# Kernel tuning notes

Hardware: AMD Instinct MI355X
Metric: run time of the kernel (lower is better)

Reference implementation:

```python
import jax, jax.numpy as jnp
import numpy as np

N, F, P, O, E = 20000, 8, 12, 32, 320000


def setup_inputs() -> dict:
    key = jax.random.key(0)
    ks = jax.random.split(key, 18)
    g = lambda k, shape: (jax.random.normal(k, shape, jnp.float32) * 0.1)
    x = jax.random.normal(ks[0], (N, F, P), jnp.float32)
    edge_index = jax.random.randint(ks[1], (2, E), 0, N, dtype=jnp.int32)
    return {
        "x": x,
        "edge_index": edge_index,
        # GCNConv weights/biases for update (z), reset (r), candidate (h) gates
        "Wz": g(ks[2], (F, O)), "bz": g(ks[3], (O,)),
        "Wr": g(ks[4], (F, O)), "br": g(ks[5], (O,)),
        "Wh": g(ks[6], (F, O)), "bh": g(ks[7], (O,)),
        # GRU linear layers (torch.nn.Linear: y = x @ W.T + b), in=2*O, out=O
        "lz_w": g(ks[8], (O, 2 * O)), "lz_b": g(ks[9], (O,)),
        "lr_w": g(ks[10], (O, 2 * O)), "lr_b": g(ks[11], (O,)),
        "lh_w": g(ks[12], (O, 2 * O)), "lh_b": g(ks[13], (O,)),
        # temporal attention logits over periods
        "att": g(ks[14], (P,)),
        # final Linear(32 -> window_size)
        "out_w": g(ks[15], (P, O)), "out_b": g(ks[16], (P,)),
    }


def reference(x, edge_index, Wz, bz, Wr, br, Wh, bh,
              lz_w, lz_b, lr_w, lr_b, lh_w, lh_b, att, out_w, out_b):
    n = x.shape[0]
    # gcn_norm with self-loops: norm_e = d^-1/2[src] * d^-1/2[dst]
    loop = jnp.arange(n, dtype=edge_index.dtype)
    src = jnp.concatenate([edge_index[0], loop])
    dst = jnp.concatenate([edge_index[1], loop])
    deg = jax.ops.segment_sum(jnp.ones(src.shape[0], x.dtype), dst, num_segments=n)
    dinv = jnp.where(deg > 0, deg ** -0.5, 0.0)
    norm = dinv[src] * dinv[dst]  # [E+n]

    def gcn(xp, W, b):
        # xp: [n, P, F] -> [n, P, O]; GCNConv: D^-1/2 (A+I) D^-1/2 (X W) + b
        h = jnp.einsum('npf,fo->npo', xp, W)
        msg = h[src] * norm[:, None, None]  # [E+n, P, O]
        return jax.ops.segment_sum(msg, dst, num_segments=n) + b

    xp = jnp.transpose(x, (0, 2, 1))  # [n, P, F]
    # A3TGCN does NOT carry H across periods (H stays initial zeros), so all
    # periods are independent GRU steps from H = 0 and can be batched.
    H = jnp.zeros(xp.shape[:2] + (O,), x.dtype)
    Z = jax.nn.sigmoid(jnp.concatenate([gcn(xp, Wz, bz), H], -1) @ lz_w.T + lz_b)
    R = jax.nn.sigmoid(jnp.concatenate([gcn(xp, Wr, br), H], -1) @ lr_w.T + lr_b)
    Ht = jnp.tanh(jnp.concatenate([gcn(xp, Wh, bh), H * R], -1) @ lh_w.T + lh_b)
    Hp = Z * H + (1.0 - Z) * Ht  # [n, P, O]
    probs = jax.nn.softmax(att)
    Hacc = jnp.einsum('npo,p->no', Hp, probs)  # attention-weighted sum
    return jax.nn.relu(Hacc) @ out_w.T + out_b  # [n, window_size]
```

## Files before the change

### kernel.cpp

```cpp
#include <hip/hip_runtime.h>
#include <math.h>

#define FP 96
#define SLOT 64
#define NPB 8
#define GBLK 128
#define PBLK 256
#define POISON ((int)0xAAAAAAAA)

__device__ __forceinline__ unsigned f2bf_bits(float f) {
    unsigned u = __float_as_uint(f);
    return (u + 0x7fffu + ((u >> 16) & 1u)) >> 16;
}
__device__ __forceinline__ float bf_lo(unsigned u) { return __uint_as_float(u << 16); }
__device__ __forceinline__ float bf_hi(unsigned u) { return __uint_as_float(u & 0xffff0000u); }

__device__ __forceinline__ int cnt_decode(int v) {
    return ((unsigned)v >= 0xAA000000u) ? v - POISON : v;
}

__global__ void k_hist_fold(const int* __restrict__ ei, int E,
                            int* __restrict__ cnt, int* __restrict__ bucket,
                            const float* __restrict__ Wz, const float* __restrict__ bz,
                            const float* __restrict__ Wh, const float* __restrict__ bh,
                            const float* __restrict__ lz_w, const float* __restrict__ lz_b,
                            const float* __restrict__ lh_w, const float* __restrict__ lh_b,
                            const float* __restrict__ att, const float* __restrict__ out_w,
                            const float* __restrict__ out_b, float* __restrict__ cst) {
    int b = blockIdx.x, t = threadIdx.x;
    if (b == gridDim.x - 1) {
        int f = t >> 5, o = t & 31;
        float sz = 0.f, sh = 0.f;
        for (int j = 0; j < 32; ++j) {
            sz += Wz[f * 32 + j] * lz_w[o * 64 + j];
            sh += Wh[f * 32 + j] * lh_w[o * 64 + j];
        }
        cst[t]       = sz;
        cst[256 + t] = sh;
        if (t < 32) {
            float a = lz_b[t], c = lh_b[t];
            for (int j = 0; j < 32; ++j) {
                a += bz[j] * lz_w[t * 64 + j];
                c += bh[j] * lh_w[t * 64 + j];
            }
            cst[512 + t] = a;
            cst[544 + t] = c;
        }
        if (t < 12) {
            float m = -1e30f;
            for (int p = 0; p < 12; ++p) m = fmaxf(m, att[p]);
            float s = 0.f;
            for (int p = 0; p < 12; ++p) s += expf(att[p] - m);
            cst[576 + t] = expf(att[t] - m) / s;
        }
        for (int i = t; i < 384; i += PBLK)
            cst[588 + (i & 31) * 12 + (i >> 5)] = out_w[i];
        if (t < 12) cst[972 + t] = out_b[t];
        return;
    }
    int e = b * PBLK + t;
    if (e >= E) return;
    int src = ei[e], dst = ei[E + e];
    int old = atomicAdd(cnt + dst, 1);
    int pos = cnt_decode(old);
    if (pos < SLOT) bucket[(size_t)dst * SLOT + pos] = src;
}

__global__ void k_convert(const float* __restrict__ x, const int* __restrict__ cnt,
                          unsigned* __restrict__ xb, int N) {
    int i = blockIdx.x * blockDim.x + threadIdx.x;
    if (i >= (N + 1) * 12) return;
    int n = i / 12;
    if (n == N) {
        ((uint4*)xb)[i] = make_uint4(0u, 0u, 0u, 0u);
        return;
    }
    int deg = cnt_decode(cnt[n]);
    float w = rsqrtf((float)(deg + 1));
    const float4* x4 = (const float4*)x;
    float4 a = x4[i * 2], c = x4[i * 2 + 1];
    uint4 r;
    r.x = f2bf_bits(w * a.x) | (f2bf_bits(w * a.y) << 16);
    r.y = f2bf_bits(w * a.z) | (f2bf_bits(w * a.w) << 16);
    r.z = f2bf_bits(w * c.x) | (f2bf_bits(w * c.y) << 16);
    r.w = f2bf_bits(w * c.z) | (f2bf_bits(w * c.w) << 16);
    ((uint4*)xb)[i] = r;
}

__device__ __forceinline__ void load_batch(uint4* P, const uint4* __restrict__ xrow,
                                           const int* list, int k) {
#pragma unroll
    for (int u = 0; u < 8; ++u) P[u] = xrow[list[u] * 12 + k];
}
__device__ __forceinline__ void acc_batch(float* acc, const uint4* C) {
    acc[0] += ((bf_lo(C[0].x) + bf_lo(C[1].x)) + (bf_lo(C[2].x) + bf_lo(C[3].x)))
            + ((bf_lo(C[4].x) + bf_lo(C[5].x)) + (bf_lo(C[6].x) + bf_lo(C[7].x)));
    acc[1] += ((bf_hi(C[0].x) + bf_hi(C[1].x)) + (bf_hi(C[2].x) + bf_hi(C[3].x)))
            + ((bf_hi(C[4].x) + bf_hi(C[5].x)) + (bf_hi(C[6].x) + bf_hi(C[7].x)));
    acc[2] += ((bf_lo(C[0].y) + bf_lo(C[1].y)) + (bf_lo(C[2].y) + bf_lo(C[3].y)))
            + ((bf_lo(C[4].y) + bf_lo(C[5].y)) + (bf_lo(C[6].y) + bf_lo(C[7].y)));
    acc[3] += ((bf_hi(C[0].y) + bf_hi(C[1].y)) + (bf_hi(C[2].y) + bf_hi(C[3].y)))
            + ((bf_hi(C[4].y) + bf_hi(C[5].y)) + (bf_hi(C[6].y) + bf_hi(C[7].y)));
    acc[4] += ((bf_lo(C[0].z) + bf_lo(C[1].z)) + (bf_lo(C[2].z) + bf_lo(C[3].z)))
            + ((bf_lo(C[4].z) + bf_lo(C[5].z)) + (bf_lo(C[6].z) + bf_lo(C[7].z)));
    acc[5] += ((bf_hi(C[0].z) + bf_hi(C[1].z)) + (bf_hi(C[2].z) + bf_hi(C[3].z)))
            + ((bf_hi(C[4].z) + bf_hi(C[5].z)) + (bf_hi(C[6].z) + bf_hi(C[7].z)));
    acc[6] += ((bf_lo(C[0].w) + bf_lo(C[1].w)) + (bf_lo(C[2].w) + bf_lo(C[3].w)))
            + ((bf_lo(C[4].w) + bf_lo(C[5].w)) + (bf_lo(C[6].w) + bf_lo(C[7].w)));
    acc[7] += ((bf_hi(C[0].w) + bf_hi(C[1].w)) + (bf_hi(C[2].w) + bf_hi(C[3].w)))
            + ((bf_hi(C[4].w) + bf_hi(C[5].w)) + (bf_hi(C[6].w) + bf_hi(C[7].w)));
}

__global__ void __launch_bounds__(GBLK)
k_gather_gates(const unsigned* __restrict__ xb, const int* __restrict__ cnt,
               const int* __restrict__ bucket, const float* __restrict__ cst,
               float* __restrict__ out, int N) {
    __shared__ float sy[NPB][FP + 4];
    __shared__ float shr[NPB][32];
    __shared__ float scst[984];
    __shared__ int   sbuck[NPB][72];
    __shared__ int   sdeg[NPB];
    int t = threadIdx.x;
    int n0 = blockIdx.x * NPB;
    const uint4* xrow = (const uint4*)xb;

    int nl = 0, k = 0, n = N;
    uint4 self = make_uint4(0u, 0u, 0u, 0u);
    if (t < NPB * 12) {
        nl = t / 12; k = t - nl * 12; n = n0 + nl;
        if (n < N) self = xrow[n * 12 + k];
    }
    if (t < NPB) sdeg[t] = (n0 + t < N) ? cnt_decode(cnt[n0 + t]) : 0;
    {
        int nd = t >> 4, q = t & 15, nn = n0 + nd;
        if (nn < N) *(int4*)&sbuck[nd][q * 4] =
            ((const int4*)(bucket + (size_t)nn * SLOT))[q];
    }
    for (int i = t; i < 984; i += GBLK) scst[i] = cst[i];
    __syncthreads();
    if (t < NPB * 8) {
        int nnl = t >> 3, q = t & 7;
        int d = min(sdeg[nnl], SLOT);
        int degp = (d + 7) & ~7; if (degp < 8) degp = 8;
        int pos = d + q;
        if (pos < degp) sbuck[nnl][pos] = N;
    }
    __syncthreads();

    if (t < NPB * 12 && n < N) {
        int c = sdeg[nl];
        int d = min(c, SLOT);
        int degp = (d + 7) & ~7; if (degp < 8) degp = 8;
        int nb = degp >> 3;
        int nA = (nb + 1) >> 1;
        int nB = nb - nA;
        const int* list = sbuck[nl];
        float acc[8] = {bf_lo(self.x), bf_hi(self.x), bf_lo(self.y), bf_hi(self.y),
                        bf_lo(self.z), bf_hi(self.z), bf_lo(self.w), bf_hi(self.w)};
        uint4 A[8], B[8];
        load_batch(A, xrow, list, k);
        if (nB > 0) load_batch(B, xrow, list + nA * 8, k);
        for (int i = 0; i < nA; ++i) {
            uint4 CA[8];
#pragma unroll
            for (int u = 0; u < 8; ++u) CA[u] = A[u];
            if (i + 1 < nA) load_batch(A, xrow, list + (i + 1) * 8, k);
            acc_batch(acc, CA);
            if (i < nB) {
                uint4 CB[8];
#pragma unroll
                for (int u = 0; u < 8; ++u) CB[u] = B[u];
                if (i + 1 < nB) load_batch(B, xrow, list + (nA + i + 1) * 8, k);
                acc_batch(acc, CB);
            }
        }
        float di = rsqrtf((float)(c + 1));
#pragma unroll
        for (int i = 0; i < 8; ++i) sy[nl][k * 8 + i] = di * acc[i];
    }
    __syncthreads();

    int o = t & 31;
#pragma unroll
    for (int it = 0; it < 2; ++it) {
        int local = (t >> 5) + it * 4, nn = n0 + local;
        if (nn < N) {
            float cz = scst[512 + o], ch = scst[544 + o];
            float hacc = 0.f;
#pragma unroll
            for (int p = 0; p < 12; ++p) {
                float az = cz, ah = ch;
#pragma unroll
                for (int f = 0; f < 8; ++f) {
                    float xf = sy[local][f * 12 + p];
                    az += xf * scst[f * 32 + o];
                    ah += xf * scst[256 + f * 32 + o];
                }
                float Z  = 1.f / (1.f + expf(-az));
                float Ht = tanhf(ah);
                hacc += scst[576 + p] * (1.f - Z) * Ht;
            }
            shr[local][o] = fmaxf(hacc, 0.f);
        }
    }
    __syncthreads();
#pragma unroll
    for (int it = 0; it < 2; ++it) {
        int local = (t >> 5) + it * 4, nn = n0 + local;
        if (nn < N && o < 12) {
            float s = scst[972 + o];
#pragma unroll
            for (int j2 = 0; j2 < 32; ++j2)
                s += shr[local][j2] * scst[588 + j2 * 12 + o];
            out[(size_t)nn * 12 + o] = s;
        }
    }
}

extern "C" void kernel_launch(void* const* d_in, const int* in_sizes, int n_in,
                              void* d_out, int out_size, void* d_ws, size_t ws_size,
                              hipStream_t stream) {
    const float* x    = (const float*)d_in[0];
    const int*   ei   = (const int*)d_in[1];
    const float* Wz   = (const float*)d_in[2];
    const float* bz   = (const float*)d_in[3];
    const float* Wh   = (const float*)d_in[6];
    const float* bh   = (const float*)d_in[7];
    const float* lz_w = (const float*)d_in[8];
    const float* lz_b = (const float*)d_in[9];
    const float* lh_w = (const float*)d_in[12];
    const float* lh_b = (const float*)d_in[13];
    const float* att  = (const float*)d_in[14];
    const float* ow   = (const float*)d_in[15];
    const float* ob   = (const float*)d_in[16];
    float* out = (float*)d_out;

    int N = in_sizes[0] / FP;
    int E = in_sizes[1] / 2;

    int*      cnt    = (int*)d_ws;
    int*      bucket = cnt + N;
    unsigned* xb     = (unsigned*)(bucket + (size_t)N * SLOT);
    float*    cst    = (float*)(xb + (size_t)(N + 1) * 48);

    int EB = (E + PBLK - 1) / PBLK;
    k_hist_fold<<<EB + 1, PBLK, 0, stream>>>(ei, E, cnt, bucket, Wz, bz, Wh, bh,
                                             lz_w, lz_b, lh_w, lh_b, att, ow, ob, cst);
    k_convert  <<<((N + 1) * 12 + PBLK - 1) / PBLK, PBLK, 0, stream>>>(x, cnt, xb, N);
    k_gather_gates<<<(N + NPB - 1) / NPB, GBLK, 0, stream>>>(xb, cnt, bucket, cst, out, N);
}
```

Measured before the change: 140.0 us.

## Fuse bf16 conversion into histogram kernel and apply source norm during gather

The bf16 conversion of x no longer scales rows by the source degree, so it can run in the same launch as the edge histogram and constant folding. This removes one kernel launch and the serial dependency between the histogram and the conversion. The gather kernel now loads each neighbour's count and applies rsqrt(deg+1) per neighbour with FMAs. The cost is an extra random int load and rsqrt per edge in the hot gather loop, plus more register pressure. The count array grows by one entry so the padding index N can be read safely.

```diff
diff --git a/kernel.cpp b/kernel.cpp
--- a/kernel.cpp
+++ b/kernel.cpp
@@ -19,96 +19,94 @@
     return ((unsigned)v >= 0xAA000000u) ? v - POISON : v;
 }
 
-__global__ void k_hist_fold(const int* __restrict__ ei, int E,
-                            int* __restrict__ cnt, int* __restrict__ bucket,
-                            const float* __restrict__ Wz, const float* __restrict__ bz,
-                            const float* __restrict__ Wh, const float* __restrict__ bh,
-                            const float* __restrict__ lz_w, const float* __restrict__ lz_b,
-                            const float* __restrict__ lh_w, const float* __restrict__ lh_b,
-                            const float* __restrict__ att, const float* __restrict__ out_w,
-                            const float* __restrict__ out_b, float* __restrict__ cst) {
+__global__ void k_prep_all(const int* __restrict__ ei, int E, int EB, int CB,
+                           int* __restrict__ cnt, int* __restrict__ bucket,
+                           const float* __restrict__ x, unsigned* __restrict__ xb, int N,
+                           const float* __restrict__ Wz, const float* __restrict__ bz,
+                           const float* __restrict__ Wh, const float* __restrict__ bh,
+                           const float* __restrict__ lz_w, const float* __restrict__ lz_b,
+                           const float* __restrict__ lh_w, const float* __restrict__ lh_b,
+                           const float* __restrict__ att, const float* __restrict__ out_w,
+                           const float* __restrict__ out_b, float* __restrict__ cst) {
     int b = blockIdx.x, t = threadIdx.x;
-    if (b == gridDim.x - 1) {
-        int f = t >> 5, o = t & 31;
-        float sz = 0.f, sh = 0.f;
+    if (b < EB) {
+        int e = b * PBLK + t;
+        if (e >= E) return;
+        int src = ei[e], dst = ei[E + e];
+        int old = atomicAdd(cnt + dst, 1);
+        int pos = cnt_decode(old);
+        if (pos < SLOT) bucket[(size_t)dst * SLOT + pos] = src;
+        return;
+    }
+    if (b < EB + CB) {
+        int i = (b - EB) * PBLK + t;
+        if (i >= (N + 1) * 12) return;
+        if (i / 12 == N) {
+            ((uint4*)xb)[i] = make_uint4(0u, 0u, 0u, 0u);
+            return;
+        }
+        const float4* x4 = (const float4*)x;
+        float4 a = x4[i * 2], c = x4[i * 2 + 1];
+        uint4 r;
+        r.x = f2bf_bits(a.x) | (f2bf_bits(a.y) << 16);
+        r.y = f2bf_bits(a.z) | (f2bf_bits(a.w) << 16);
+        r.z = f2bf_bits(c.x) | (f2bf_bits(c.y) << 16);
+        r.w = f2bf_bits(c.z) | (f2bf_bits(c.w) << 16);
+        ((uint4*)xb)[i] = r;
+        return;
+    }
+    int f = t >> 5, o = t & 31;
+    float sz = 0.f, sh = 0.f;
+    for (int j = 0; j < 32; ++j) {
+        sz += Wz[f * 32 + j] * lz_w[o * 64 + j];
+        sh += Wh[f * 32 + j] * lh_w[o * 64 + j];
+    }
+    cst[t]       = sz;
+    cst[256 + t] = sh;
+    if (t < 32) {
+        float a = lz_b[t], c = lh_b[t];
         for (int j = 0; j < 32; ++j) {
-            sz += Wz[f * 32 + j] * lz_w[o * 64 + j];
-            sh += Wh[f * 32 + j] * lh_w[o * 64 + j];
-        }
-        cst[t]       = sz;
-        cst[256 + t] = sh;
-        if (t < 32) {
-            float a = lz_b[t], c = lh_b[t];
-            for (int j = 0; j < 32; ++j) {
-                a += bz[j] * lz_w[t * 64 + j];
-                c += bh[j] * lh_w[t * 64 + j];
-            }
-            cst[512 + t] = a;
-            cst[544 + t] = c;
-        }
-        if (t < 12) {
-            float m = -1e30f;
-            for (int p = 0; p < 12; ++p) m = fmaxf(m, att[p]);
-            float s = 0.f;
-            for (int p = 0; p < 12; ++p) s += expf(att[p] - m);
-            cst[576 + t] = expf(att[t] - m) / s;
-        }
-        for (int i = t; i < 384; i += PBLK)
-            cst[588 + (i & 31) * 12 + (i >> 5)] = out_w[i];
-        if (t < 12) cst[972 + t] = out_b[t];
-        return;
-    }
-    int e = b * PBLK + t;
-    if (e >= E) return;
-    int src = ei[e], dst = ei[E + e];
-    int old = atomicAdd(cnt + dst, 1);
-    int pos = cnt_decode(old);
-    if (pos < SLOT) bucket[(size_t)dst * SLOT + pos] = src;
-}
-
-__global__ void k_convert(const float* __restrict__ x, const int* __restrict__ cnt,
-                          unsigned* __restrict__ xb, int N) {
-    int i = blockIdx.x * blockDim.x + threadIdx.x;
-    if (i >= (N + 1) * 12) return;
-    int n = i / 12;
-    if (n == N) {
-        ((uint4*)xb)[i] = make_uint4(0u, 0u, 0u, 0u);
-        return;
-    }
-    int deg = cnt_decode(cnt[n]);
-    float w = rsqrtf((float)(deg + 1));
-    const float4* x4 = (const float4*)x;
-    float4 a = x4[i * 2], c = x4[i * 2 + 1];
-    uint4 r;
-    r.x = f2bf_bits(w * a.x) | (f2bf_bits(w * a.y) << 16);
-    r.y = f2bf_bits(w * a.z) | (f2bf_bits(w * a.w) << 16);
-    r.z = f2bf_bits(w * c.x) | (f2bf_bits(w * c.y) << 16);
-    r.w = f2bf_bits(w * c.z) | (f2bf_bits(w * c.w) << 16);
-    ((uint4*)xb)[i] = r;
-}
-
-__device__ __forceinline__ void load_batch(uint4* P, const uint4* __restrict__ xrow,
+            a += bz[j] * lz_w[t * 64 + j];
+            c += bh[j] * lh_w[t * 64 + j];
+        }
+        cst[512 + t] = a;
+        cst[544 + t] = c;
+    }
+    if (t < 12) {
+        float m = -1e30f;
+        for (int p = 0; p < 12; ++p) m = fmaxf(m, att[p]);
+        float s = 0.f;
+        for (int p = 0; p < 12; ++p) s += expf(att[p] - m);
+        cst[576 + t] = expf(att[t] - m) / s;
+    }
+    for (int i = t; i < 384; i += PBLK)
+        cst[588 + (i & 31) * 12 + (i >> 5)] = out_w[i];
+    if (t < 12) cst[972 + t] = out_b[t];
+}
+
+__device__ __forceinline__ void load_batch(uint4* P, int* pc, const uint4* __restrict__ xrow,
+                                           const int* __restrict__ cntp,
                                            const int* list, int k) {
 #pragma unroll
-    for (int u = 0; u < 8; ++u) P[u] = xrow[list[u] * 12 + k];
-}
-__device__ __forceinline__ void acc_batch(float* acc, const uint4* C) {
-    acc[0] += ((bf_lo(C[0].x) + bf_lo(C[1].x)) + (bf_lo(C[2].x) + bf_lo(C[3].x)))
-            + ((bf_lo(C[4].x) + bf_lo(C[5].x)) + (bf_lo(C[6].x) + bf_lo(C[7].x)));
-    acc[1] += ((bf_hi(C[0].x) + bf_hi(C[1].x)) + (bf_hi(C[2].x) + bf_hi(C[3].x)))
-            + ((bf_hi(C[4].x) + bf_hi(C[5].x)) + (bf_hi(C[6].x) + bf_hi(C[7].x)));
-    acc[2] += ((bf_lo(C[0].y) + bf_lo(C[1].y)) + (bf_lo(C[2].y) + bf_lo(C[3].y)))
-            + ((bf_lo(C[4].y) + bf_lo(C[5].y)) + (bf_lo(C[6].y) + bf_lo(C[7].y)));
-    acc[3] += ((bf_hi(C[0].y) + bf_hi(C[1].y)) + (bf_hi(C[2].y) + bf_hi(C[3].y)))
-            + ((bf_hi(C[4].y) + bf_hi(C[5].y)) + (bf_hi(C[6].y) + bf_hi(C[7].y)));
-    acc[4] += ((bf_lo(C[0].z) + bf_lo(C[1].z)) + (bf_lo(C[2].z) + bf_lo(C[3].z)))
-            + ((bf_lo(C[4].z) + bf_lo(C[5].z)) + (bf_lo(C[6].z) + bf_lo(C[7].z)));
-    acc[5] += ((bf_hi(C[0].z) + bf_hi(C[1].z)) + (bf_hi(C[2].z) + bf_hi(C[3].z)))
-            + ((bf_hi(C[4].z) + bf_hi(C[5].z)) + (bf_hi(C[6].z) + bf_hi(C[7].z)));
-    acc[6] += ((bf_lo(C[0].w) + bf_lo(C[1].w)) + (bf_lo(C[2].w) + bf_lo(C[3].w)))
-            + ((bf_lo(C[4].w) + bf_lo(C[5].w)) + (bf_lo(C[6].w) + bf_lo(C[7].w)));
-    acc[7] += ((bf_hi(C[0].w) + bf_hi(C[1].w)) + (bf_hi(C[2].w) + bf_hi(C[3].w)))
-            + ((bf_hi(C[4].w) + bf_hi(C[5].w)) + (bf_hi(C[6].w) + bf_hi(C[7].w)));
+    for (int u = 0; u < 8; ++u) {
+        int s = list[u];
+        pc[u] = cntp[s];
+        P[u]  = xrow[s * 12 + k];
+    }
+}
+__device__ __forceinline__ void acc_batch_w(float* acc, const uint4* C, const int* pc) {
+#pragma unroll
+    for (int u = 0; u < 8; ++u) {
+        float w = rsqrtf((float)(cnt_decode(pc[u]) + 1));
+        acc[0] = fmaf(w, bf_lo(C[u].x), acc[0]);
+        acc[1] = fmaf(w, bf_hi(C[u].x), acc[1]);
+        acc[2] = fmaf(w, bf_lo(C[u].y), acc[2]);
+        acc[3] = fmaf(w, bf_hi(C[u].y), acc[3]);
+        acc[4] = fmaf(w, bf_lo(C[u].z), acc[4]);
+        acc[5] = fmaf(w, bf_hi(C[u].z), acc[5]);
+        acc[6] = fmaf(w, bf_lo(C[u].w), acc[6]);
+        acc[7] = fmaf(w, bf_hi(C[u].w), acc[7]);
+    }
 }
 
 __global__ void __launch_bounds__(GBLK)
@@ -155,26 +153,29 @@
         int nA = (nb + 1) >> 1;
         int nB = nb - nA;
         const int* list = sbuck[nl];
-        float acc[8] = {bf_lo(self.x), bf_hi(self.x), bf_lo(self.y), bf_hi(self.y),
-                        bf_lo(self.z), bf_hi(self.z), bf_lo(self.w), bf_hi(self.w)};
+        float di = rsqrtf((float)(c + 1));
+        float acc[8] = {di * bf_lo(self.x), di * bf_hi(self.x),
+                        di * bf_lo(self.y), di * bf_hi(self.y),
+                        di * bf_lo(self.z), di * bf_hi(self.z),
+                        di * bf_lo(self.w), di * bf_hi(self.w)};
         uint4 A[8], B[8];
-        load_batch(A, xrow, list, k);
-        if (nB > 0) load_batch(B, xrow, list + nA * 8, k);
+        int   cA[8], cB[8];
+        load_batch(A, cA, xrow, cnt, list, k);
+        if (nB > 0) load_batch(B, cB, xrow, cnt, list + nA * 8, k);
         for (int i = 0; i < nA; ++i) {
-            uint4 CA[8];
-#pragma unroll
-            for (int u = 0; u < 8; ++u) CA[u] = A[u];
-            if (i + 1 < nA) load_batch(A, xrow, list + (i + 1) * 8, k);
-            acc_batch(acc, CA);
+            uint4 CA[8]; int wA[8];
+#pragma unroll
+            for (int u = 0; u < 8; ++u) { CA[u] = A[u]; wA[u] = cA[u]; }
+            if (i + 1 < nA) load_batch(A, cA, xrow, cnt, list + (i + 1) * 8, k);
+            acc_batch_w(acc, CA, wA);
             if (i < nB) {
-                uint4 CB[8];
-#pragma unroll
-                for (int u = 0; u < 8; ++u) CB[u] = B[u];
-                if (i + 1 < nB) load_batch(B, xrow, list + (nA + i + 1) * 8, k);
-                acc_batch(acc, CB);
+                uint4 CB[8]; int wB[8];
+#pragma unroll
+                for (int u = 0; u < 8; ++u) { CB[u] = B[u]; wB[u] = cB[u]; }
+                if (i + 1 < nB) load_batch(B, cB, xrow, cnt, list + (nA + i + 1) * 8, k);
+                acc_batch_w(acc, CB, wB);
             }
         }
-        float di = rsqrtf((float)(c + 1));
 #pragma unroll
         for (int i = 0; i < 8; ++i) sy[nl][k * 8 + i] = di * acc[i];
     }
@@ -239,13 +240,14 @@
     int E = in_sizes[1] / 2;
 
     int*      cnt    = (int*)d_ws;
-    int*      bucket = cnt + N;
+    int*      bucket = cnt + (N + 1);
     unsigned* xb     = (unsigned*)(bucket + (size_t)N * SLOT);
     float*    cst    = (float*)(xb + (size_t)(N + 1) * 48);
 
     int EB = (E + PBLK - 1) / PBLK;
-    k_hist_fold<<<EB + 1, PBLK, 0, stream>>>(ei, E, cnt, bucket, Wz, bz, Wh, bh,
-                                             lz_w, lz_b, lh_w, lh_b, att, ow, ob, cst);
-    k_convert  <<<((N + 1) * 12 + PBLK - 1) / PBLK, PBLK, 0, stream>>>(x, cnt, xb, N);
+    int CB = ((N + 1) * 12 + PBLK - 1) / PBLK;
+    k_prep_all<<<EB + CB + 1, PBLK, 0, stream>>>(ei, E, EB, CB, cnt, bucket, x, xb, N,
+                                                 Wz, bz, Wh, bh, lz_w, lz_b, lh_w, lh_b,
+                                                 att, ow, ob, cst);
     k_gather_gates<<<(N + NPB - 1) / NPB, GBLK, 0, stream>>>(xb, cnt, bucket, cst, out, N);
 }
```

Result: slower. 144.0 us (+2.8%).

## Split per-node neighbor gather across two thread halves and double block size

Applied to the files above, without the earlier changes.

Doubles the gather block to 256 threads and assigns two threads per (node, feature-chunk), each gathering half of the padded neighbor list into separate shared buffers that are then summed. This is meant to shorten the serial per-thread gather chain and raise memory-level parallelism in the latency-bound neighbor loads. The gate stage now runs one node per 32-thread group instead of looping twice. It costs an extra shared-memory reduction pass, a barrier, more padding to multiples of 16, and higher register and LDS pressure per block. The bucket pointer offset also shifts by one int.

```diff
diff --git a/kernel.cpp b/kernel.cpp
--- a/kernel.cpp
+++ b/kernel.cpp
@@ -4,7 +4,7 @@
 #define FP 96
 #define SLOT 64
 #define NPB 8
-#define GBLK 128
+#define GBLK 256
 #define PBLK 256
 #define POISON ((int)0xAAAAAAAA)
 
@@ -115,7 +115,7 @@
 k_gather_gates(const unsigned* __restrict__ xb, const int* __restrict__ cnt,
                const int* __restrict__ bucket, const float* __restrict__ cst,
                float* __restrict__ out, int N) {
-    __shared__ float sy[NPB][FP + 4];
+    __shared__ float sy2[2][NPB][FP + 4];
     __shared__ float shr[NPB][32];
     __shared__ float scst[984];
     __shared__ int   sbuck[NPB][72];
@@ -124,37 +124,41 @@
     int n0 = blockIdx.x * NPB;
     const uint4* xrow = (const uint4*)xb;
 
-    int nl = 0, k = 0, n = N;
+    int nl = 0, h = 0, k = 0, n = N;
+    if (t < NPB * 24) {
+        nl = t / 24; int l24 = t - nl * 24;
+        h = l24 / 12; k = l24 - h * 12;
+        n = n0 + nl;
+    }
     uint4 self = make_uint4(0u, 0u, 0u, 0u);
-    if (t < NPB * 12) {
-        nl = t / 12; k = t - nl * 12; n = n0 + nl;
-        if (n < N) self = xrow[n * 12 + k];
-    }
+    if (t < NPB * 24 && h == 0 && n < N) self = xrow[n * 12 + k];
+
     if (t < NPB) sdeg[t] = (n0 + t < N) ? cnt_decode(cnt[n0 + t]) : 0;
-    {
+    if (t < NPB * 16) {
         int nd = t >> 4, q = t & 15, nn = n0 + nd;
         if (nn < N) *(int4*)&sbuck[nd][q * 4] =
             ((const int4*)(bucket + (size_t)nn * SLOT))[q];
     }
     for (int i = t; i < 984; i += GBLK) scst[i] = cst[i];
     __syncthreads();
-    if (t < NPB * 8) {
-        int nnl = t >> 3, q = t & 7;
+    if (t < NPB * 16) {
+        int nnl = t >> 4, q = t & 15;
         int d = min(sdeg[nnl], SLOT);
-        int degp = (d + 7) & ~7; if (degp < 8) degp = 8;
+        int degp = (d + 15) & ~15; if (degp < 16) degp = 16;
         int pos = d + q;
         if (pos < degp) sbuck[nnl][pos] = N;
     }
     __syncthreads();
 
-    if (t < NPB * 12 && n < N) {
+    if (t < NPB * 24 && n < N) {
         int c = sdeg[nl];
         int d = min(c, SLOT);
-        int degp = (d + 7) & ~7; if (degp < 8) degp = 8;
-        int nb = degp >> 3;
+        int degp = (d + 15) & ~15; if (degp < 16) degp = 16;
+        int half_len = degp >> 1;
+        int nb = half_len >> 3;
         int nA = (nb + 1) >> 1;
         int nB = nb - nA;
-        const int* list = sbuck[nl];
+        const int* list = sbuck[nl] + h * half_len;
         float acc[8] = {bf_lo(self.x), bf_hi(self.x), bf_lo(self.y), bf_hi(self.y),
                         bf_lo(self.z), bf_hi(self.z), bf_lo(self.w), bf_hi(self.w)};
         uint4 A[8], B[8];
@@ -176,14 +180,18 @@
         }
         float di = rsqrtf((float)(c + 1));
 #pragma unroll
-        for (int i = 0; i < 8; ++i) sy[nl][k * 8 + i] = di * acc[i];
+        for (int i = 0; i < 8; ++i) sy2[h][nl][k * 8 + i] = di * acc[i];
+    }
+    __syncthreads();
+    for (int i = t; i < NPB * FP; i += GBLK) {
+        int nnl = i / FP, j = i - nnl * FP;
+        sy2[0][nnl][j] += sy2[1][nnl][j];
     }
     __syncthreads();
 
     int o = t & 31;
-#pragma unroll
-    for (int it = 0; it < 2; ++it) {
-        int local = (t >> 5) + it * 4, nn = n0 + local;
+    {
+        int local = t >> 5, nn = n0 + local;
         if (nn < N) {
             float cz = scst[512 + o], ch = scst[544 + o];
             float hacc = 0.f;
@@ -192,7 +200,7 @@
                 float az = cz, ah = ch;
 #pragma unroll
                 for (int f = 0; f < 8; ++f) {
-                    float xf = sy[local][f * 12 + p];
+                    float xf = sy2[0][local][f * 12 + p];
                     az += xf * scst[f * 32 + o];
                     ah += xf * scst[256 + f * 32 + o];
                 }
@@ -204,9 +212,8 @@
         }
     }
     __syncthreads();
-#pragma unroll
-    for (int it = 0; it < 2; ++it) {
-        int local = (t >> 5) + it * 4, nn = n0 + local;
+    {
+        int local = t >> 5, nn = n0 + local;
         if (nn < N && o < 12) {
             float s = scst[972 + o];
 #pragma unroll
@@ -239,7 +246,7 @@
     int E = in_sizes[1] / 2;
 
     int*      cnt    = (int*)d_ws;
-    int*      bucket = cnt + N;
+    int*      bucket = cnt + (N + 1);
     unsigned* xb     = (unsigned*)(bucket + (size_t)N * SLOT);
     float*    cst    = (float*)(xb + (size_t)(N + 1) * 48);
 
```

New measurement: 141.6 us. About the same (+1.1%).
